# Performance work log

Measured on AMD Instinct MI355X. Metric: run time of the kernel, lower is better.

Reference implementation:

```python
import jax, jax.numpy as jnp
import numpy as np

K = 7          # window kernel size
PAD = 3        # padding so out spatial == in spatial (stride=1, dilation=1)
BN_EPS = 1e-5


def conv1x1(x, w, b):
    # x: (b,c,h,w), w: (o,c), b: (o,)
    return jnp.einsum('bchw,oc->bohw', x, w) + b[None, :, None, None]


def bn_relu(x, bn):
    # bn: (4, C) rows = gamma, beta, running_mean, running_var (inference-mode BN)
    g, bta, m, v = bn[0], bn[1], bn[2], bn[3]
    scale = g / jnp.sqrt(v + BN_EPS)
    y = (x - m[None, :, None, None]) * scale[None, :, None, None] + bta[None, :, None, None]
    return jax.nn.relu(y)


def extract_patches(x):
    # Equivalent of F.unfold(x, K, padding=PAD, stride=1) reshaped to (b, C, K*K, H, W).
    # Ordering matches torch: channel major, kernel positions row-major.
    b, c, h, w = x.shape
    xp = jnp.pad(x, ((0, 0), (0, 0), (PAD, PAD), (PAD, PAD)))
    ps = [xp[:, :, i:i + h, j:j + w] for i in range(K) for j in range(K)]
    return jnp.stack(ps, axis=2)  # (b, c, K*K, h, w)


def setup_inputs() -> dict:
    key = jax.random.key(0)
    ks = jax.random.split(key, 20)
    Cin, Ck, Cv, Co = 256, 64, 128, 256
    b, h, w = 2, 96, 96

    def wgt(k, o, c):
        return jax.random.normal(k, (o, c), jnp.float32) * 0.05

    def bias(k, o):
        return jax.random.normal(k, (o,), jnp.float32) * 0.02

    def bn(k, c):
        g = 1.0 + 0.1 * jax.random.normal(k, (c,), jnp.float32)
        bta = 0.1 * jax.random.normal(jax.random.fold_in(k, 1), (c,), jnp.float32)
        m = 0.05 * jax.random.normal(jax.random.fold_in(k, 2), (c,), jnp.float32)
        v = 1.0 + 0.1 * jax.random.uniform(jax.random.fold_in(k, 3), (c,), jnp.float32)
        return jnp.stack([g, bta, m, v])  # (4, c)

    return {
        'x': jax.random.normal(ks[0], (b, Cin, h, w), jnp.float32),
        'fk_w1': wgt(ks[1], Ck, Cin), 'fk_b1': bias(ks[2], Ck), 'fk_bn1': bn(ks[3], Ck),
        'fk_w2': wgt(ks[4], Ck, Ck), 'fk_b2': bias(ks[5], Ck), 'fk_bn2': bn(ks[6], Ck),
        'fq_w1': wgt(ks[7], Ck, Cin), 'fq_b1': bias(ks[8], Ck), 'fq_bn1': bn(ks[9], Ck),
        'fq_w2': wgt(ks[10], Ck, Ck), 'fq_b2': bias(ks[11], Ck), 'fq_bn2': bn(ks[12], Ck),
        'fv_w': wgt(ks[13], Cv, Cin), 'fv_b': bias(ks[14], Cv),
        'W_w': wgt(ks[15], Co, Cv), 'W_b': bias(ks[16], Co),
    }


def reference(x, fk_w1, fk_b1, fk_bn1, fk_w2, fk_b2, fk_bn2,
              fq_w1, fq_b1, fq_bn1, fq_w2, fq_b2, fq_bn2,
              fv_w, fv_b, W_w, W_b):
    # scale=1 -> no pooling. stride=1, dilation=1, pad=3, k=7 -> out spatial == in spatial.
    value = conv1x1(x, fv_w, fv_b)                       # (b, Cv, H, W)
    unfold_value = extract_patches(value)                # (b, Cv, 49, H, W)

    k1 = bn_relu(conv1x1(x, fk_w1, fk_b1), fk_bn1)
    key = bn_relu(conv1x1(k1, fk_w2, fk_b2), fk_bn2)     # (b, Ck, H, W)
    unfold_key = extract_patches(key)                    # (b, Ck, 49, H, W)

    q1 = bn_relu(conv1x1(x, fq_w1, fq_b1), fq_bn1)
    query = bn_relu(conv1x1(q1, fq_w2, fq_b2), fq_bn2)   # (b, Ck, H, W)
    # start_index = dilation*(k//2) - padding = 0; stride=1 -> query slice is identity.

    sim = jnp.sum(unfold_key * query[:, :, None], axis=1, keepdims=True)  # (b,1,49,H,W)
    sim = jax.nn.softmax(sim, axis=2)
    context = jnp.sum(sim * unfold_value, axis=2)        # (b, Cv, H, W)
    context = conv1x1(context, W_w, W_b)                 # (b, Co, H, W)
    # F.interpolate to (h, w) with align_corners=True is identity (same size).
    return context
```

## Files before the change

kernel.cpp:

```cpp
#include <hip/hip_runtime.h>
#include <hip/hip_bf16.h>

typedef _Float16 f16;
typedef _Float16 f16x4 __attribute__((ext_vector_type(4)));
typedef _Float16 f16x8 __attribute__((ext_vector_type(8)));
typedef float f32x4 __attribute__((ext_vector_type(4)));

#define HH 96
#define WW 96
#define HWs 9216
#define BN_EPS 1e-5f

#define OFF_ACT1 0u
#define OFF_ACT2 4718592u

__global__ __launch_bounds__(256) void conv12(
    const float* __restrict__ x,
    const float* __restrict__ fv_w, const float* __restrict__ fk_w1, const float* __restrict__ fq_w1,
    const float* __restrict__ fk_w2, const float* __restrict__ fq_w2,
    const float* __restrict__ fv_b,
    const float* __restrict__ fk_b1, const float* __restrict__ fk_bn1,
    const float* __restrict__ fq_b1, const float* __restrict__ fq_bn1,
    const float* __restrict__ fk_b2, const float* __restrict__ fk_bn2,
    const float* __restrict__ fq_b2, const float* __restrict__ fq_bn2,
    f16* __restrict__ act1, f16* __restrict__ act2)
{
  __shared__ f16 As[32 * 40];
  __shared__ f16 Bs[256 * 40];
  __shared__ f16 kqs[2][32 * 72];
  const int tid = threadIdx.x;
  const int l = tid & 63, w = tid >> 6;
  const int bb = blockIdx.y;
  const int p0 = blockIdx.x * 32;
  const int lrow = l & 15, lk = (l >> 4) * 8;

  f32x4 acc[2][4];
#pragma unroll
  for (int i = 0; i < 2; i++)
#pragma unroll
    for (int j = 0; j < 4; j++) acc[i][j] = (f32x4){0.f, 0.f, 0.f, 0.f};

  const int spx = tid & 31, skg = tid >> 5;
#pragma unroll 1
  for (int ks = 0; ks < 8; ks++) {
    f16x4 av;
#pragma unroll
    for (int j = 0; j < 4; j++)
      av[j] = (f16)x[((size_t)bb * 256 + ks * 32 + skg * 4 + j) * HWs + p0 + spx];
    *(f16x4*)&As[spx * 40 + skg * 4] = av;
#pragma unroll
    for (int it = 0; it < 4; it++) {
      int tt = it * 256 + tid;
      int row = tt >> 2, seg = tt & 3;
      const float* srcp;
      if (it < 2)      srcp = fv_w  + (size_t)row * 256;
      else if (it == 2) srcp = fk_w1 + (size_t)(row - 128) * 256;
      else              srcp = fq_w1 + (size_t)(row - 192) * 256;
      float4 u0 = *(const float4*)&srcp[ks * 32 + seg * 8];
      float4 u1 = *(const float4*)&srcp[ks * 32 + seg * 8 + 4];
      f16x8 h = {(f16)u0.x, (f16)u0.y, (f16)u0.z, (f16)u0.w,
                 (f16)u1.x, (f16)u1.y, (f16)u1.z, (f16)u1.w};
      *(f16x8*)&Bs[row * 40 + seg * 8] = h;
    }
    __syncthreads();
    f16x8 a[2], b[4];
#pragma unroll
    for (int mi = 0; mi < 2; mi++) a[mi] = *(const f16x8*)&As[(mi * 16 + lrow) * 40 + lk];
#pragma unroll
    for (int nj = 0; nj < 4; nj++) b[nj] = *(const f16x8*)&Bs[(w * 64 + nj * 16 + lrow) * 40 + lk];
#pragma unroll
    for (int mi = 0; mi < 2; mi++)
#pragma unroll
      for (int nj = 0; nj < 4; nj++)
        acc[mi][nj] = __builtin_amdgcn_mfma_f32_16x16x32_f16(a[mi], b[nj], acc[mi][nj], 0, 0, 0);
    __syncthreads();
  }

#pragma unroll
  for (int nj = 0; nj < 4; nj++) {
    int cout = w * 64 + nj * 16 + lrow;
    float s, t;
    if (w < 2) { s = 1.0f; t = fv_b[cout]; }
    else {
      int j = nj * 16 + lrow;
      const float* bn = (w == 2) ? fk_bn1 : fq_bn1;
      const float* bs = (w == 2) ? fk_b1 : fq_b1;
      float g = bn[j], be = bn[64 + j], m = bn[128 + j], v = bn[192 + j];
      s = g * rsqrtf(v + BN_EPS); t = (bs[j] - m) * s + be;
    }
#pragma unroll
    for (int mi = 0; mi < 2; mi++)
#pragma unroll
      for (int r = 0; r < 4; r++) {
        int px = mi * 16 + (l >> 4) * 4 + r;
        float v = acc[mi][nj][r] * s + t;
        if (w < 2) {
          act1[((size_t)bb * HWs + p0 + px) * 128 + cout] = (f16)v;
        } else {
          kqs[w - 2][px * 72 + (nj * 16 + lrow)] = (f16)fmaxf(v, 0.f);
        }
      }
  }
  __syncthreads();

  const int sel = w >> 1, half = w & 1;
  const float* W2s = sel ? fq_w2 : fk_w2;
  f32x4 acc2[2][2];
#pragma unroll
  for (int i = 0; i < 2; i++)
#pragma unroll
    for (int j = 0; j < 2; j++) acc2[i][j] = (f32x4){0.f, 0.f, 0.f, 0.f};
#pragma unroll
  for (int ks = 0; ks < 2; ks++) {
    f16x8 a2[2], b2[2];
#pragma unroll
    for (int mi = 0; mi < 2; mi++)
      a2[mi] = *(const f16x8*)&kqs[sel][(mi * 16 + lrow) * 72 + ks * 32 + lk];
#pragma unroll
    for (int nj = 0; nj < 2; nj++) {
      const float* wp = &W2s[(size_t)(half * 32 + nj * 16 + lrow) * 64 + ks * 32 + lk];
      float4 u0 = *(const float4*)&wp[0];
      float4 u1 = *(const float4*)&wp[4];
      b2[nj] = (f16x8){(f16)u0.x, (f16)u0.y, (f16)u0.z, (f16)u0.w,
                       (f16)u1.x, (f16)u1.y, (f16)u1.z, (f16)u1.w};
    }
#pragma unroll
    for (int mi = 0; mi < 2; mi++)
#pragma unroll
      for (int nj = 0; nj < 2; nj++)
        acc2[mi][nj] = __builtin_amdgcn_mfma_f32_16x16x32_f16(a2[mi], b2[nj], acc2[mi][nj], 0, 0, 0);
  }
#pragma unroll
  for (int nj = 0; nj < 2; nj++) {
    int j2 = half * 32 + nj * 16 + lrow;
    int c2 = sel * 64 + j2;
    const float* bn = sel ? fq_bn2 : fk_bn2;
    const float* bs = sel ? fq_b2 : fk_b2;
    float g = bn[j2], be = bn[64 + j2], m = bn[128 + j2], v = bn[192 + j2];
    float s = g * rsqrtf(v + BN_EPS), t = (bs[j2] - m) * s + be;
#pragma unroll
    for (int mi = 0; mi < 2; mi++)
#pragma unroll
      for (int r = 0; r < 4; r++) {
        int px = mi * 16 + (l >> 4) * 4 + r;
        float vv = fmaxf(acc2[mi][nj][r] * s + t, 0.f);
        act2[((size_t)bb * HWs + p0 + px) * 128 + c2] = (f16)vv;
      }
  }
}

__global__ __launch_bounds__(256) void attn_final(const f16* __restrict__ act1,
                                                  const f16* __restrict__ act2,
                                                  const float* __restrict__ W_w,
                                                  const float* __restrict__ W_b,
                                                  float* __restrict__ out)
{
  __shared__ f16 Qs[32 * 72];
  __shared__ f16 Ks[144 * 72];
  __shared__ f16 Vs[144 * 136];
  __shared__ float Ps[32 * 52];
  const int tid = threadIdx.x;
  const int l = tid & 63, w = tid >> 6;
  const int bb = blockIdx.z;
  const int x0 = blockIdx.x * 8, y0 = blockIdx.y * 4;
  const f16* a2 = act2 + (size_t)bb * HWs * 128;
  const f16* a1 = act1 + (size_t)bb * HWs * 128;
  const int lrow = l & 15, lk = (l >> 4) * 8;

  {
    int q = tid >> 3, seg = tid & 7;
    int gp = (y0 + (q >> 3)) * WW + x0 + (q & 7);
    *(f16x8*)&Qs[q * 72 + seg * 8] = *(const f16x8*)&a2[(size_t)gp * 128 + 64 + seg * 8];
  }
  for (int t = tid; t < 1152; t += 256) {
    int kk = t >> 3, seg = t & 7;
    int ky = (kk * 4682) >> 16, kx = kk - 14 * ky;
    int gy = y0 - 3 + ky, gx = x0 - 3 + kx;
    f16x8 v = {(f16)0, (f16)0, (f16)0, (f16)0, (f16)0, (f16)0, (f16)0, (f16)0};
    if (kk < 140 && (unsigned)gy < (unsigned)HH && (unsigned)gx < (unsigned)WW)
      v = *(const f16x8*)&a2[((size_t)(gy * WW + gx)) * 128 + seg * 8];
    *(f16x8*)&Ks[kk * 72 + seg * 8] = v;
  }
  for (int t = tid; t < 2304; t += 256) {
    int kk = t >> 4, seg = t & 15;
    int ky = (kk * 4682) >> 16, kx = kk - 14 * ky;
    int gy = y0 - 3 + ky, gx = x0 - 3 + kx;
    f16x8 v = {(f16)0, (f16)0, (f16)0, (f16)0, (f16)0, (f16)0, (f16)0, (f16)0};
    if (kk < 140 && (unsigned)gy < (unsigned)HH && (unsigned)gx < (unsigned)WW)
      v = *(const f16x8*)&a1[((size_t)(gy * WW + gx)) * 128 + seg * 8];
    *(f16x8*)&Vs[kk * 136 + seg * 8] = v;
  }
  __syncthreads();

  if (w < 2) {
    f32x4 sc[9];
#pragma unroll
    for (int nj = 0; nj < 9; nj++) sc[nj] = (f32x4){0.f, 0.f, 0.f, 0.f};
#pragma unroll
    for (int ks = 0; ks < 2; ks++) {
      f16x8 aq = *(const f16x8*)&Qs[(w * 16 + lrow) * 72 + ks * 32 + lk];
#pragma unroll
      for (int nj = 0; nj < 9; nj++) {
        f16x8 bk = *(const f16x8*)&Ks[(nj * 16 + lrow) * 72 + ks * 32 + lk];
        sc[nj] = __builtin_amdgcn_mfma_f32_16x16x32_f16(aq, bk, sc[nj], 0, 0, 0);
      }
    }
    const int r0 = w * 16 + (l >> 4) * 4;
#pragma unroll
    for (int nj = 0; nj < 9; nj++) {
      int c = nj * 16 + lrow;
      int ky = (c * 4682) >> 16, kx = c - 14 * ky;
#pragma unroll
      for (int r = 0; r < 4; r++) {
        int row = r0 + r;
        int qy = (row >> 3), qx = row & 7;
        bool valid = (c < 140) && ((unsigned)(ky - qy) < 7u) && ((unsigned)(kx - qx) < 7u);
        if (!valid) sc[nj][r] = -1e30f;
      }
    }
    float mx[4], sm[4], inv[4];
#pragma unroll
    for (int r = 0; r < 4; r++) {
      mx[r] = -1e30f;
#pragma unroll
      for (int nj = 0; nj < 9; nj++) mx[r] = fmaxf(mx[r], sc[nj][r]);
    }
#pragma unroll
    for (int off = 1; off < 16; off <<= 1)
#pragma unroll
      for (int r = 0; r < 4; r++) mx[r] = fmaxf(mx[r], __shfl_xor(mx[r], off));
#pragma unroll
    for (int r = 0; r < 4; r++) sm[r] = 0.f;
#pragma unroll
    for (int nj = 0; nj < 9; nj++)
#pragma unroll
      for (int r = 0; r < 4; r++) {
        float e = __expf(sc[nj][r] - mx[r]);
        sc[nj][r] = e; sm[r] += e;
      }
#pragma unroll
    for (int off = 1; off < 16; off <<= 1)
#pragma unroll
      for (int r = 0; r < 4; r++) sm[r] += __shfl_xor(sm[r], off);
#pragma unroll
    for (int r = 0; r < 4; r++) inv[r] = 1.0f / sm[r];
#pragma unroll
    for (int nj = 0; nj < 9; nj++) {
      int c = nj * 16 + lrow;
      int ky = (c * 4682) >> 16, kx = c - 14 * ky;
#pragma unroll
      for (int r = 0; r < 4; r++) {
        int row = r0 + r;
        int qy = (row >> 3), qx = row & 7;
        int dy = ky - qy, dx = kx - qx;
        if (c < 140 && ((unsigned)dy < 7u) && ((unsigned)dx < 7u))
          Ps[row * 52 + dy * 7 + dx] = sc[nj][r] * inv[r];
      }
    }
  }
  __syncthreads();

  const int q = tid >> 3, c8 = tid & 7;
  const int qy = q >> 3, qx = q & 7;
  const int ch0 = c8 * 16;
  float acc[16];
#pragma unroll
  for (int i = 0; i < 16; i++) acc[i] = 0.f;
#pragma unroll
  for (int dy = 0; dy < 7; dy++)
#pragma unroll
    for (int dx = 0; dx < 7; dx++) {
      float p = Ps[q * 52 + dy * 7 + dx];
      int kk = (qy + dy) * 14 + qx + dx;
      const f16* vp = &Vs[kk * 136 + ch0];
      f16x8 v0 = *(const f16x8*)&vp[0];
      f16x8 v1 = *(const f16x8*)&vp[8];
#pragma unroll
      for (int j = 0; j < 8; j++) {
        acc[j] += (float)v0[j] * p;
        acc[8 + j] += (float)v1[j] * p;
      }
    }
  __syncthreads();

  {
    f16x8 o0, o1;
#pragma unroll
    for (int j = 0; j < 8; j++) { o0[j] = (f16)acc[j]; o1[j] = (f16)acc[8 + j]; }
    *(f16x8*)&Vs[q * 136 + ch0] = o0;
    *(f16x8*)&Vs[q * 136 + ch0 + 8] = o1;
  }
  __syncthreads();

  f32x4 fac[4][2];
#pragma unroll
  for (int i = 0; i < 4; i++)
#pragma unroll
    for (int j = 0; j < 2; j++) fac[i][j] = (f32x4){0.f, 0.f, 0.f, 0.f};
#pragma unroll
  for (int ks = 0; ks < 4; ks++) {
    f16x8 a3[4], b3[2];
#pragma unroll
    for (int mi = 0; mi < 4; mi++) {
      const float* wp = &W_w[(size_t)(w * 64 + mi * 16 + lrow) * 128 + ks * 32 + lk];
      float4 u0 = *(const float4*)&wp[0];
      float4 u1 = *(const float4*)&wp[4];
      a3[mi] = (f16x8){(f16)u0.x, (f16)u0.y, (f16)u0.z, (f16)u0.w,
                       (f16)u1.x, (f16)u1.y, (f16)u1.z, (f16)u1.w};
    }
#pragma unroll
    for (int nj = 0; nj < 2; nj++)
      b3[nj] = *(const f16x8*)&Vs[(nj * 16 + lrow) * 136 + ks * 32 + lk];
#pragma unroll
    for (int mi = 0; mi < 4; mi++)
#pragma unroll
      for (int nj = 0; nj < 2; nj++)
        fac[mi][nj] = __builtin_amdgcn_mfma_f32_16x16x32_f16(a3[mi], b3[nj], fac[mi][nj], 0, 0, 0);
  }
#pragma unroll
  for (int mi = 0; mi < 4; mi++)
#pragma unroll
    for (int r = 0; r < 4; r++) {
      int cout = w * 64 + mi * 16 + (l >> 4) * 4 + r;
      float bias = W_b[cout];
#pragma unroll
      for (int nj = 0; nj < 2; nj++) {
        int px = nj * 16 + lrow;
        int gp = (y0 + (px >> 3)) * WW + x0 + (px & 7);
        out[((size_t)bb * 256 + cout) * HWs + gp] = fac[mi][nj][r] + bias;
      }
    }
}

extern "C" void kernel_launch(void* const* d_in, const int* in_sizes, int n_in,
                              void* d_out, int out_size, void* d_ws, size_t ws_size,
                              hipStream_t stream) {
  (void)in_sizes; (void)n_in; (void)out_size; (void)ws_size;
  const float* x      = (const float*)d_in[0];
  const float* fk_w1  = (const float*)d_in[1];
  const float* fk_b1  = (const float*)d_in[2];
  const float* fk_bn1 = (const float*)d_in[3];
  const float* fk_w2  = (const float*)d_in[4];
  const float* fk_b2  = (const float*)d_in[5];
  const float* fk_bn2 = (const float*)d_in[6];
  const float* fq_w1  = (const float*)d_in[7];
  const float* fq_b1  = (const float*)d_in[8];
  const float* fq_bn1 = (const float*)d_in[9];
  const float* fq_w2  = (const float*)d_in[10];
  const float* fq_b2  = (const float*)d_in[11];
  const float* fq_bn2 = (const float*)d_in[12];
  const float* fv_w   = (const float*)d_in[13];
  const float* fv_b   = (const float*)d_in[14];
  const float* W_w    = (const float*)d_in[15];
  const float* W_b    = (const float*)d_in[16];
  char* wsb = (char*)d_ws;
  float* out = (float*)d_out;

  f16* act1 = (f16*)(wsb + OFF_ACT1);
  f16* act2 = (f16*)(wsb + OFF_ACT2);

  conv12<<<dim3(288, 2), dim3(256), 0, stream>>>(
      x, fv_w, fk_w1, fq_w1, fk_w2, fq_w2,
      fv_b, fk_b1, fk_bn1, fq_b1, fq_bn1,
      fk_b2, fk_bn2, fq_b2, fq_bn2, act1, act2);

  attn_final<<<dim3(12, 24, 2), dim3(256), 0, stream>>>(act1, act2, W_w, W_b, out);
}
```

Before: 156.8 us.

## Enlarge attention tile to 8x8 and double-buffer conv weight staging

The attention kernel now handles an 8x8 query tile per block instead of 8x4. This cuts halo overhead on the key/value loads (196 vs 140 window positions for twice the queries) and puts all four waves on the score MFMAs rather than two. V is prefetched into registers and written to a shared buffer that aliases the Q/K storage after the softmax, which keeps LDS usage in check. In conv12, the whole x tile is staged once and the weight slices are double-buffered, removing one barrier per k-step. The cost is heavier register pressure (13 V vectors, 32 accumulators, 13 score tiles), which may lower occupancy, and the attention grid is halved.

New measurement: 164.0 us. +4.5%, slower.

```diff
diff --git a/kernel.cpp b/kernel.cpp
--- a/kernel.cpp
+++ b/kernel.cpp
@@ -25,8 +25,8 @@
     const float* __restrict__ fq_b2, const float* __restrict__ fq_bn2,
     f16* __restrict__ act1, f16* __restrict__ act2)
 {
-  __shared__ f16 As[32 * 40];
-  __shared__ f16 Bs[256 * 40];
+  __shared__ f16 As[32 * 264];
+  __shared__ f16 Bs[2][256 * 40];
   __shared__ f16 kqs[2][32 * 72];
   const int tid = threadIdx.x;
   const int l = tid & 63, w = tid >> 6;
@@ -34,46 +34,57 @@
   const int p0 = blockIdx.x * 32;
   const int lrow = l & 15, lk = (l >> 4) * 8;
 
-  f32x4 acc[2][4];
-#pragma unroll
-  for (int i = 0; i < 2; i++)
-#pragma unroll
-    for (int j = 0; j < 4; j++) acc[i][j] = (f32x4){0.f, 0.f, 0.f, 0.f};
-
-  const int spx = tid & 31, skg = tid >> 5;
-#pragma unroll 1
-  for (int ks = 0; ks < 8; ks++) {
+  const int spx = tid & 31, scg = tid >> 5;
+#pragma unroll
+  for (int it = 0; it < 8; ++it) {
+    int ch = it * 32 + scg * 4;
     f16x4 av;
 #pragma unroll
     for (int j = 0; j < 4; j++)
-      av[j] = (f16)x[((size_t)bb * 256 + ks * 32 + skg * 4 + j) * HWs + p0 + spx];
-    *(f16x4*)&As[spx * 40 + skg * 4] = av;
+      av[j] = (f16)x[((size_t)bb * 256 + ch + j) * HWs + p0 + spx];
+    *(f16x4*)&As[spx * 264 + ch] = av;
+  }
+
+  auto stageW = [&](int ks, int bf) {
 #pragma unroll
     for (int it = 0; it < 4; it++) {
       int tt = it * 256 + tid;
       int row = tt >> 2, seg = tt & 3;
       const float* srcp;
-      if (it < 2)      srcp = fv_w  + (size_t)row * 256;
+      if (it < 2)       srcp = fv_w  + (size_t)row * 256;
       else if (it == 2) srcp = fk_w1 + (size_t)(row - 128) * 256;
       else              srcp = fq_w1 + (size_t)(row - 192) * 256;
       float4 u0 = *(const float4*)&srcp[ks * 32 + seg * 8];
       float4 u1 = *(const float4*)&srcp[ks * 32 + seg * 8 + 4];
       f16x8 h = {(f16)u0.x, (f16)u0.y, (f16)u0.z, (f16)u0.w,
                  (f16)u1.x, (f16)u1.y, (f16)u1.z, (f16)u1.w};
-      *(f16x8*)&Bs[row * 40 + seg * 8] = h;
-    }
+      *(f16x8*)&Bs[bf][row * 40 + seg * 8] = h;
+    }
+  };
+
+  f32x4 acc[2][4];
+#pragma unroll
+  for (int i = 0; i < 2; i++)
+#pragma unroll
+    for (int j = 0; j < 4; j++) acc[i][j] = (f32x4){0.f, 0.f, 0.f, 0.f};
+
+  stageW(0, 0);
+#pragma unroll 1
+  for (int ks = 0; ks < 8; ks++) {
     __syncthreads();
+    if (ks < 7) stageW(ks + 1, (ks + 1) & 1);
     f16x8 a[2], b[4];
 #pragma unroll
-    for (int mi = 0; mi < 2; mi++) a[mi] = *(const f16x8*)&As[(mi * 16 + lrow) * 40 + lk];
-#pragma unroll
-    for (int nj = 0; nj < 4; nj++) b[nj] = *(const f16x8*)&Bs[(w * 64 + nj * 16 + lrow) * 40 + lk];
+    for (int mi = 0; mi < 2; mi++)
+      a[mi] = *(const f16x8*)&As[(mi * 16 + lrow) * 264 + ks * 32 + lk];
+#pragma unroll
+    for (int nj = 0; nj < 4; nj++)
+      b[nj] = *(const f16x8*)&Bs[ks & 1][(w * 64 + nj * 16 + lrow) * 40 + lk];
 #pragma unroll
     for (int mi = 0; mi < 2; mi++)
 #pragma unroll
       for (int nj = 0; nj < 4; nj++)
         acc[mi][nj] = __builtin_amdgcn_mfma_f32_16x16x32_f16(a[mi], b[nj], acc[mi][nj], 0, 0, 0);
-    __syncthreads();
   }
 
 #pragma unroll
@@ -155,117 +166,124 @@
                                                   const float* __restrict__ W_b,
                                                   float* __restrict__ out)
 {
-  __shared__ f16 Qs[32 * 72];
-  __shared__ f16 Ks[144 * 72];
-  __shared__ f16 Vs[144 * 136];
-  __shared__ float Ps[32 * 52];
+  __shared__ float Ps[64 * 52];
+  __shared__ f16 buf[208 * 136];
   const int tid = threadIdx.x;
   const int l = tid & 63, w = tid >> 6;
   const int bb = blockIdx.z;
-  const int x0 = blockIdx.x * 8, y0 = blockIdx.y * 4;
+  const int x0 = blockIdx.x * 8, y0 = blockIdx.y * 8;
   const f16* a2 = act2 + (size_t)bb * HWs * 128;
   const f16* a1 = act1 + (size_t)bb * HWs * 128;
+  f16* Qs = buf;
+  f16* Ks = buf + 64 * 72;
   const int lrow = l & 15, lk = (l >> 4) * 8;
 
-  {
-    int q = tid >> 3, seg = tid & 7;
+#pragma unroll
+  for (int it = 0; it < 2; it++) {
+    int t = it * 256 + tid;
+    int q = t >> 3, seg = t & 7;
     int gp = (y0 + (q >> 3)) * WW + x0 + (q & 7);
     *(f16x8*)&Qs[q * 72 + seg * 8] = *(const f16x8*)&a2[(size_t)gp * 128 + 64 + seg * 8];
   }
-  for (int t = tid; t < 1152; t += 256) {
+  for (int t = tid; t < 1664; t += 256) {
     int kk = t >> 3, seg = t & 7;
     int ky = (kk * 4682) >> 16, kx = kk - 14 * ky;
     int gy = y0 - 3 + ky, gx = x0 - 3 + kx;
     f16x8 v = {(f16)0, (f16)0, (f16)0, (f16)0, (f16)0, (f16)0, (f16)0, (f16)0};
-    if (kk < 140 && (unsigned)gy < (unsigned)HH && (unsigned)gx < (unsigned)WW)
+    if (kk < 196 && (unsigned)gy < (unsigned)HH && (unsigned)gx < (unsigned)WW)
       v = *(const f16x8*)&a2[((size_t)(gy * WW + gx)) * 128 + seg * 8];
     *(f16x8*)&Ks[kk * 72 + seg * 8] = v;
   }
-  for (int t = tid; t < 2304; t += 256) {
-    int kk = t >> 4, seg = t & 15;
+  f16x8 vv[13];
+  const int vk0 = tid >> 4, vseg = tid & 15;
+#pragma unroll
+  for (int it = 0; it < 13; ++it) {
+    int kk = vk0 + it * 16;
     int ky = (kk * 4682) >> 16, kx = kk - 14 * ky;
     int gy = y0 - 3 + ky, gx = x0 - 3 + kx;
     f16x8 v = {(f16)0, (f16)0, (f16)0, (f16)0, (f16)0, (f16)0, (f16)0, (f16)0};
-    if (kk < 140 && (unsigned)gy < (unsigned)HH && (unsigned)gx < (unsigned)WW)
-      v = *(const f16x8*)&a1[((size_t)(gy * WW + gx)) * 128 + seg * 8];
-    *(f16x8*)&Vs[kk * 136 + seg * 8] = v;
-  }
-  __syncthreads();
-
-  if (w < 2) {
-    f32x4 sc[9];
-#pragma unroll
-    for (int nj = 0; nj < 9; nj++) sc[nj] = (f32x4){0.f, 0.f, 0.f, 0.f};
-#pragma unroll
-    for (int ks = 0; ks < 2; ks++) {
-      f16x8 aq = *(const f16x8*)&Qs[(w * 16 + lrow) * 72 + ks * 32 + lk];
-#pragma unroll
-      for (int nj = 0; nj < 9; nj++) {
-        f16x8 bk = *(const f16x8*)&Ks[(nj * 16 + lrow) * 72 + ks * 32 + lk];
-        sc[nj] = __builtin_amdgcn_mfma_f32_16x16x32_f16(aq, bk, sc[nj], 0, 0, 0);
-      }
-    }
-    const int r0 = w * 16 + (l >> 4) * 4;
-#pragma unroll
-    for (int nj = 0; nj < 9; nj++) {
-      int c = nj * 16 + lrow;
-      int ky = (c * 4682) >> 16, kx = c - 14 * ky;
-#pragma unroll
-      for (int r = 0; r < 4; r++) {
-        int row = r0 + r;
-        int qy = (row >> 3), qx = row & 7;
-        bool valid = (c < 140) && ((unsigned)(ky - qy) < 7u) && ((unsigned)(kx - qx) < 7u);
-        if (!valid) sc[nj][r] = -1e30f;
-      }
-    }
-    float mx[4], sm[4], inv[4];
+    if (kk < 196 && (unsigned)gy < (unsigned)HH && (unsigned)gx < (unsigned)WW)
+      v = *(const f16x8*)&a1[((size_t)(gy * WW + gx)) * 128 + vseg * 8];
+    vv[it] = v;
+  }
+  __syncthreads();
+
+  f32x4 sc[13];
+#pragma unroll
+  for (int nj = 0; nj < 13; nj++) sc[nj] = (f32x4){0.f, 0.f, 0.f, 0.f};
+#pragma unroll
+  for (int ks = 0; ks < 2; ks++) {
+    f16x8 aq = *(const f16x8*)&Qs[(w * 16 + lrow) * 72 + ks * 32 + lk];
+#pragma unroll
+    for (int nj = 0; nj < 13; nj++) {
+      f16x8 bk = *(const f16x8*)&Ks[(nj * 16 + lrow) * 72 + ks * 32 + lk];
+      sc[nj] = __builtin_amdgcn_mfma_f32_16x16x32_f16(aq, bk, sc[nj], 0, 0, 0);
+    }
+  }
+  const int r0 = w * 16 + (l >> 4) * 4;
+#pragma unroll
+  for (int nj = 0; nj < 13; nj++) {
+    int c = nj * 16 + lrow;
+    int ky = (c * 4682) >> 16, kx = c - 14 * ky;
 #pragma unroll
     for (int r = 0; r < 4; r++) {
-      mx[r] = -1e30f;
-#pragma unroll
-      for (int nj = 0; nj < 9; nj++) mx[r] = fmaxf(mx[r], sc[nj][r]);
-    }
-#pragma unroll
-    for (int off = 1; off < 16; off <<= 1)
-#pragma unroll
-      for (int r = 0; r < 4; r++) mx[r] = fmaxf(mx[r], __shfl_xor(mx[r], off));
-#pragma unroll
-    for (int r = 0; r < 4; r++) sm[r] = 0.f;
-#pragma unroll
-    for (int nj = 0; nj < 9; nj++)
-#pragma unroll
-      for (int r = 0; r < 4; r++) {
-        float e = __expf(sc[nj][r] - mx[r]);
-        sc[nj][r] = e; sm[r] += e;
-      }
-#pragma unroll
-    for (int off = 1; off < 16; off <<= 1)
-#pragma unroll
-      for (int r = 0; r < 4; r++) sm[r] += __shfl_xor(sm[r], off);
-#pragma unroll
-    for (int r = 0; r < 4; r++) inv[r] = 1.0f / sm[r];
-#pragma unroll
-    for (int nj = 0; nj < 9; nj++) {
-      int c = nj * 16 + lrow;
-      int ky = (c * 4682) >> 16, kx = c - 14 * ky;
-#pragma unroll
-      for (int r = 0; r < 4; r++) {
-        int row = r0 + r;
-        int qy = (row >> 3), qx = row & 7;
-        int dy = ky - qy, dx = kx - qx;
-        if (c < 140 && ((unsigned)dy < 7u) && ((unsigned)dx < 7u))
-          Ps[row * 52 + dy * 7 + dx] = sc[nj][r] * inv[r];
-      }
-    }
-  }
-  __syncthreads();
-
-  const int q = tid >> 3, c8 = tid & 7;
+      int qy = (r0 + r) >> 3, qx = (r0 + r) & 7;
+      bool valid = ((unsigned)(ky - qy) < 7u) && ((unsigned)(kx - qx) < 7u);
+      if (!valid) sc[nj][r] = -1e30f;
+    }
+  }
+  float mx[4], sm[4], inv[4];
+#pragma unroll
+  for (int r = 0; r < 4; r++) {
+    mx[r] = -1e30f;
+#pragma unroll
+    for (int nj = 0; nj < 13; nj++) mx[r] = fmaxf(mx[r], sc[nj][r]);
+  }
+#pragma unroll
+  for (int off = 1; off < 16; off <<= 1)
+#pragma unroll
+    for (int r = 0; r < 4; r++) mx[r] = fmaxf(mx[r], __shfl_xor(mx[r], off));
+#pragma unroll
+  for (int r = 0; r < 4; r++) sm[r] = 0.f;
+#pragma unroll
+  for (int nj = 0; nj < 13; nj++)
+#pragma unroll
+    for (int r = 0; r < 4; r++) {
+      float e = __expf(sc[nj][r] - mx[r]);
+      sc[nj][r] = e; sm[r] += e;
+    }
+#pragma unroll
+  for (int off = 1; off < 16; off <<= 1)
+#pragma unroll
+    for (int r = 0; r < 4; r++) sm[r] += __shfl_xor(sm[r], off);
+#pragma unroll
+  for (int r = 0; r < 4; r++) inv[r] = 1.0f / sm[r];
+#pragma unroll
+  for (int nj = 0; nj < 13; nj++) {
+    int c = nj * 16 + lrow;
+    int ky = (c * 4682) >> 16, kx = c - 14 * ky;
+#pragma unroll
+    for (int r = 0; r < 4; r++) {
+      int qy = (r0 + r) >> 3, qx = (r0 + r) & 7;
+      int dy = ky - qy, dx = kx - qx;
+      if (((unsigned)dy < 7u) && ((unsigned)dx < 7u))
+        Ps[(r0 + r) * 52 + dy * 7 + dx] = sc[nj][r] * inv[r];
+    }
+  }
+  __syncthreads();
+
+  f16* Vs = buf;
+#pragma unroll
+  for (int it = 0; it < 13; ++it)
+    *(f16x8*)&Vs[(size_t)(vk0 + it * 16) * 136 + vseg * 8] = vv[it];
+  __syncthreads();
+
+  const int q = tid >> 2;
   const int qy = q >> 3, qx = q & 7;
-  const int ch0 = c8 * 16;
-  float acc[16];
-#pragma unroll
-  for (int i = 0; i < 16; i++) acc[i] = 0.f;
+  const int ch0 = (tid & 3) * 32;
+  float acc[32];
+#pragma unroll
+  for (int i = 0; i < 32; i++) acc[i] = 0.f;
 #pragma unroll
   for (int dy = 0; dy < 7; dy++)
 #pragma unroll
@@ -273,33 +291,33 @@
       float p = Ps[q * 52 + dy * 7 + dx];
       int kk = (qy + dy) * 14 + qx + dx;
       const f16* vp = &Vs[kk * 136 + ch0];
-      f16x8 v0 = *(const f16x8*)&vp[0];
-      f16x8 v1 = *(const f16x8*)&vp[8];
-#pragma unroll
-      for (int j = 0; j < 8; j++) {
-        acc[j] += (float)v0[j] * p;
-        acc[8 + j] += (float)v1[j] * p;
+#pragma unroll
+      for (int s = 0; s < 4; s++) {
+        f16x8 v = *(const f16x8*)&vp[s * 8];
+#pragma unroll
+        for (int j = 0; j < 8; j++) acc[s * 8 + j] += (float)v[j] * p;
       }
     }
   __syncthreads();
 
-  {
-    f16x8 o0, o1;
-#pragma unroll
-    for (int j = 0; j < 8; j++) { o0[j] = (f16)acc[j]; o1[j] = (f16)acc[8 + j]; }
-    *(f16x8*)&Vs[q * 136 + ch0] = o0;
-    *(f16x8*)&Vs[q * 136 + ch0 + 8] = o1;
-  }
-  __syncthreads();
-
-  f32x4 fac[4][2];
+  f16* ctxs = buf;
+#pragma unroll
+  for (int s = 0; s < 4; s++) {
+    f16x8 o;
+#pragma unroll
+    for (int j = 0; j < 8; j++) o[j] = (f16)acc[s * 8 + j];
+    *(f16x8*)&ctxs[q * 136 + ch0 + s * 8] = o;
+  }
+  __syncthreads();
+
+  f32x4 fac[4][4];
 #pragma unroll
   for (int i = 0; i < 4; i++)
 #pragma unroll
-    for (int j = 0; j < 2; j++) fac[i][j] = (f32x4){0.f, 0.f, 0.f, 0.f};
+    for (int j = 0; j < 4; j++) fac[i][j] = (f32x4){0.f, 0.f, 0.f, 0.f};
 #pragma unroll
   for (int ks = 0; ks < 4; ks++) {
-    f16x8 a3[4], b3[2];
+    f16x8 a3[4], b3[4];
 #pragma unroll
     for (int mi = 0; mi < 4; mi++) {
       const float* wp = &W_w[(size_t)(w * 64 + mi * 16 + lrow) * 128 + ks * 32 + lk];
@@ -309,12 +327,12 @@
                        (f16)u1.x, (f16)u1.y, (f16)u1.z, (f16)u1.w};
     }
 #pragma unroll
-    for (int nj = 0; nj < 2; nj++)
-      b3[nj] = *(const f16x8*)&Vs[(nj * 16 + lrow) * 136 + ks * 32 + lk];
+    for (int nj = 0; nj < 4; nj++)
+      b3[nj] = *(const f16x8*)&ctxs[(nj * 16 + lrow) * 136 + ks * 32 + lk];
 #pragma unroll
     for (int mi = 0; mi < 4; mi++)
 #pragma unroll
-      for (int nj = 0; nj < 2; nj++)
+      for (int nj = 0; nj < 4; nj++)
         fac[mi][nj] = __builtin_amdgcn_mfma_f32_16x16x32_f16(a3[mi], b3[nj], fac[mi][nj], 0, 0, 0);
   }
 #pragma unroll
@@ -324,7 +342,7 @@
       int cout = w * 64 + mi * 16 + (l >> 4) * 4 + r;
       float bias = W_b[cout];
 #pragma unroll
-      for (int nj = 0; nj < 2; nj++) {
+      for (int nj = 0; nj < 4; nj++) {
         int px = nj * 16 + lrow;
         int gp = (y0 + (px >> 3)) * WW + x0 + (px & 7);
         out[((size_t)bb * 256 + cout) * HWs + gp] = fac[mi][nj][r] + bias;
@@ -364,5 +382,5 @@
       fv_b, fk_b1, fk_bn1, fq_b1, fq_bn1,
       fk_b2, fk_bn2, fq_b2, fq_bn2, act1, act2);
 
-  attn_final<<<dim3(12, 24, 2), dim3(256), 0, stream>>>(act1, act2, W_w, W_b, out);
+  attn_final<<<dim3(12, 12, 2), dim3(256), 0, stream>>>(act1, act2, W_w, W_b, out);
 }
```
